# Performance work log

Measured on AMD Instinct MI355X. Metric: run time of the kernel, lower is better.

## Reference

```python
import jax, jax.numpy as jnp
import numpy as np

PI = 3.141592653589793
DET_THRESHOLD = 0.25
MAX_DET = 100
REG_HEAD = 4
DEPTH_MEAN = 28.01  # smoke_coder.depth_ref[0]
DIM_REF = (3.88, 1.63, 1.53)  # smoke_coder.dim_ref[0] (l, h, w)


def setup_inputs() -> dict:
    key = jax.random.key(0)
    k1, k2, k3, k4 = jax.random.split(key, 4)
    B, C, H, W = 32, 3, 256, 832  # stride-4 feature map of 3328x1024 images
    pred_heatmap = jax.random.uniform(k1, (B, C, H, W), dtype=jnp.float32)
    pred_regression = jax.random.normal(k2, (B, C + 1, H, W), dtype=jnp.float32) * 0.1  # REG_HEAD=4 channels
    trans_mat = jnp.tile(jnp.array([[0.25, 0.0, 0.0], [0.0, 0.25, 0.0], [0.0, 0.0, 1.0]], jnp.float32), (B, 1, 1))
    K_mat = jnp.tile(jnp.array([[2100.0, 0.0, 1664.0], [0.0, 2100.0, 512.0], [0.0, 0.0, 1.0]], jnp.float32), (B, 1, 1))
    size = jnp.tile(jnp.array([3328.0, 1024.0], jnp.float32), (B, 1))  # (img_w, img_h)
    h_cam = jax.random.uniform(k3, (B,), jnp.float32, 1.4, 2.0)
    dimensions = jax.random.uniform(k4, (B, 3), jnp.float32, 1.5, 4.0)
    return dict(pred_heatmap=pred_heatmap, pred_regression=pred_regression, trans_mat=trans_mat,
                K_mat=K_mat, size=size, h_cam=h_cam, dimensions=dimensions)


def reference(pred_heatmap, pred_regression, trans_mat, K_mat, size, h_cam, dimensions):
    B, C, H, W = pred_heatmap.shape
    K = MAX_DET
    # ---- nms_hm: 3x3 max-pool, keep local maxima ----
    hmax = jax.lax.reduce_window(pred_heatmap, -jnp.inf, jax.lax.max, (1, 1, 3, 3), (1, 1, 1, 1), 'SAME')
    heat = pred_heatmap * (hmax == pred_heatmap).astype(pred_heatmap.dtype)
    # ---- select_topk: per-class topk then global topk ----
    scores_c, inds_c = jax.lax.top_k(heat.reshape(B, C, H * W), K)  # [B,C,K]
    ys_c = (inds_c // W).astype(jnp.float32)
    xs_c = (inds_c % W).astype(jnp.float32)
    scores, topk_ind = jax.lax.top_k(scores_c.reshape(B, C * K), K)  # [B,K]
    clses = (topk_ind // K).astype(jnp.float32)
    inds = jnp.take_along_axis(inds_c.reshape(B, C * K), topk_ind, axis=1)
    ys = jnp.take_along_axis(ys_c.reshape(B, C * K), topk_ind, axis=1)
    xs = jnp.take_along_axis(xs_c.reshape(B, C * K), topk_ind, axis=1)
    feat = pred_regression.reshape(B, REG_HEAD, H * W).transpose(0, 2, 1)  # [B,HW,R]
    pois = jnp.take_along_axis(feat, inds[:, :, None], axis=1).reshape(-1, REG_HEAD)  # [B*K,R]
    log_dv_delta = pois[:, 0]
    off_u = pois[:, 1]
    ori = pois[:, 2:]
    # ---- feature points -> image points via inverse affine ----
    pts = jnp.stack([xs.reshape(-1), ys.reshape(-1)], axis=1)
    pts = pts + jnp.stack([off_u, jnp.zeros_like(off_u)], axis=1)
    pts_h = jnp.concatenate([pts, jnp.ones((pts.shape[0], 1), pts.dtype)], axis=1)  # [N,3]
    obj = jnp.repeat(jnp.arange(B), K)
    trans_inv = jnp.linalg.inv(trans_mat)[obj]  # [N,3,3]
    img_pts = jnp.einsum('nij,nj->ni', trans_inv, pts_h)[:, :2]
    # ---- per-object camera params ----
    Ks = K_mat[obj]
    h = h_cam[obj]
    kd = dimensions[obj]
    fx, fy, cx = Ks[:, 0, 0], Ks[:, 1, 1], Ks[:, 0, 2]
    dim_ref = jnp.array(DIM_REF, jnp.float32)
    dims = jnp.where(jnp.isfinite(kd), kd, dim_ref[None, :])
    # ---- geometric depth decode ----
    h_ref = h - dims[:, 1] / 2.0
    log_dv_ref = jnp.log(jnp.clip(fy * jnp.abs(h_ref), 1e-7, None) / DEPTH_MEAN)
    log_dv = jnp.clip(log_dv_ref + log_dv_delta, -4.0, 8.0)
    depths = jnp.clip(fy * jnp.abs(h_ref) * jnp.exp(-log_dv), 0.5, 120.0)
    px = (img_pts[:, 0] - cx) * depths / fx
    locs = jnp.stack([px, h, depths], axis=1)  # [N,3]
    # ---- decode_orientation (SMOKE) ----
    rays = jnp.arctan(locs[:, 0] / (locs[:, 2] + 1e-7))
    alphas = jnp.arctan(ori[:, 0] / (ori[:, 1] + 1e-7))
    alphas = alphas + jnp.where(ori[:, 1] >= 0, -PI / 2, PI / 2)
    rotys = alphas + rays
    rotys = jnp.where(rotys > PI, rotys - 2 * PI, rotys)
    rotys = jnp.where(rotys < -PI, rotys + 2 * PI, rotys)
    # ---- encode_box2d: build 3D corners, rotate, project, clamp ----
    cos, sin = jnp.cos(rotys), jnp.sin(rotys)
    cx8 = jnp.array([-0.5, 0.5, 0.5, 0.5, 0.5, -0.5, -0.5, -0.5], jnp.float32)
    cy8 = jnp.array([-1.0, -1.0, 0.0, 0.0, -1.0, -1.0, 0.0, 0.0], jnp.float32)
    cz8 = jnp.array([-0.5, -0.5, -0.5, 0.5, 0.5, 0.5, 0.5, -0.5], jnp.float32)
    xc = dims[:, 0:1] * cx8  # l
    yc = dims[:, 1:2] * cy8  # h
    zc = dims[:, 2:3] * cz8  # w
    bx = cos[:, None] * xc + sin[:, None] * zc
    bz = -sin[:, None] * xc + cos[:, None] * zc
    box3d = jnp.stack([bx, yc, bz], axis=1) + locs[:, :, None]  # [N,3,8]
    proj = jnp.einsum('nij,njk->nik', Ks, box3d)
    uv = proj[:, :2, :] / proj[:, 2:3, :]
    img_w = size.reshape(-1)[0]
    img_h = size.reshape(-1)[1]
    xmins = jnp.clip(jnp.min(uv[:, 0, :], axis=1), 0.0, img_w)
    xmaxs = jnp.clip(jnp.max(uv[:, 0, :], axis=1), 0.0, img_w)
    ymins = jnp.clip(jnp.min(uv[:, 1, :], axis=1), 0.0, img_h)
    ymaxs = jnp.clip(jnp.max(uv[:, 1, :], axis=1), 0.0, img_h)
    box2d = jnp.stack([xmins, ymins, xmaxs, ymaxs], axis=1)
    pred_dims = jnp.roll(dims, -1, axis=1)  # (l,h,w)->(h,w,l)
    result = jnp.concatenate([clses.reshape(-1, 1), alphas[:, None], box2d, pred_dims, locs,
                              rotys[:, None], scores.reshape(-1, 1)], axis=1)  # [N,14]
    # fixed-shape equivalent of boolean filtering: zero out rows below threshold
    keep = (result[:, -1] > DET_THRESHOLD).astype(result.dtype)
    return result * keep[:, None]
```

## Files before the change

kernel.cpp:

```cpp
#include <hip/hip_runtime.h>
#include <math.h>

#define B_ 32
#define C_ 3
#define H_ 256
#define W_ 832
#define HW_ (H_*W_)
#define K_ 100
#define RPB 16
#define PARTS (H_/RPB)
#define NLOAD (W_/4)
#define BLK 256
#define CAP 2048
#define NCAND (C_*PARTS*K_)
#define NB 2048
#define TIE_CAP 128
#define SEL_PASSES 6

typedef unsigned long long ull;
struct DetRec { float score; int cls; unsigned hw; };

template<int N>
__device__ inline void bitonic_sort_desc(ull* s) {
    for (int k = 2; k <= N; k <<= 1) {
        for (int j = k >> 1; j > 0; j >>= 1) {
            __syncthreads();
            for (int i = threadIdx.x; i < N; i += BLK) {
                int ixj = i ^ j;
                if (ixj > i) {
                    ull a = s[i], b = s[ixj];
                    bool up = ((i & k) == 0);
                    if (up ? (a < b) : (a > b)) { s[i] = b; s[ixj] = a; }
                }
            }
        }
    }
    __syncthreads();
}

__device__ inline void find_digit(const unsigned* __restrict__ hist,
                                  unsigned* __restrict__ wtot,
                                  const int kneed,
                                  int* __restrict__ d_s,
                                  int* __restrict__ krem_s,
                                  int* __restrict__ m_s) {
    const int tid = threadIdx.x;
    const int lane = tid & 63;
    const int wid = tid >> 6;
    unsigned l[8];
    unsigned Ls = 0;
    #pragma unroll
    for (int j = 0; j < 8; ++j) { l[j] = hist[tid * 8 + j]; Ls += l[j]; }
    unsigned x = Ls;
    #pragma unroll
    for (int off = 1; off < 64; off <<= 1) {
        unsigned y = __shfl_down(x, off);
        if (lane + off < 64) x += y;
    }
    if (lane == 0) wtot[wid] = x;
    __syncthreads();
    unsigned tail = 0;
    #pragma unroll
    for (int w = 0; w < 4; ++w) if (w > wid) tail += wtot[w];
    unsigned s = x - Ls + tail;
    #pragma unroll
    for (int j = 7; j >= 0; --j) {
        const unsigned Sj = s + l[j];
        if (Sj >= (unsigned)kneed && s < (unsigned)kneed) {
            *d_s = tid * 8 + j;
            *krem_s = kneed - (int)s;
            *m_s = (int)l[j];
        }
        s = Sj;
    }
    __syncthreads();
}

__device__ inline void select_topk(const ull* __restrict__ buf, const int cnt,
                                   ull* __restrict__ dst,
                                   unsigned* __restrict__ hist,
                                   ull* __restrict__ tie,
                                   unsigned* __restrict__ wtot,
                                   int* __restrict__ sh) {
    const int tid = threadIdx.x;
    if (tid == 0) sh[0] = 0;
    int kneed = K_;
    int pshift = 0;
    ull prefix = 0;
    for (int pass = 0; pass < SEL_PASSES; ++pass) {
        const int rs = 53 - 11 * pass;
        const int shift = (rs > 0) ? rs : 0;
        #pragma unroll
        for (int j = 0; j < NB / BLK; ++j) hist[tid + j * BLK] = 0u;
        if (tid == 0) sh[1] = 0;
        __syncthreads();
        for (int i = tid; i < cnt; i += BLK) {
            const ull key = buf[i];
            if (pass > 0 && (key >> pshift) != prefix) continue;
            atomicAdd(&hist[(unsigned)(key >> shift) & 2047u], 1u);
        }
        __syncthreads();
        find_digit(hist, wtot, kneed, &sh[2], &sh[3], &sh[4]);
        const int d = sh[2], krem = sh[3], m = sh[4];
        const bool last = (m <= TIE_CAP) || (pass == SEL_PASSES - 1);
        for (int i = tid; i < cnt; i += BLK) {
            const ull key = buf[i];
            if (pass > 0 && (key >> pshift) != prefix) continue;
            const int dg = (int)((unsigned)(key >> shift) & 2047u);
            if (dg > d) {
                dst[atomicAdd(&sh[0], 1)] = key;
            } else if (last && dg == d) {
                const int p = atomicAdd(&sh[1], 1);
                if (p < TIE_CAP) tie[p] = key;
            }
        }
        __syncthreads();
        if (last) {
            const int n1 = K_ - krem;
            if (sh[1] <= TIE_CAP) {
                const int mm = sh[1];
                for (int i = tid; i < mm; i += BLK) {
                    const ull key = tie[i];
                    int r = 0;
                    for (int j = 0; j < mm; ++j) r += (tie[j] > key) ? 1 : 0;
                    if (r < krem) dst[n1 + r] = key;
                }
            } else {
                for (int i = tid; i < krem; i += BLK) dst[n1 + i] = tie[0];
            }
            __syncthreads();
            return;
        }
        prefix = (prefix << 11) | (ull)(unsigned)d;
        pshift = shift;
        kneed = krem;
    }
}

union TopkShared {
    float vm[2][W_];
    unsigned hist[NB];
};

__global__ void __launch_bounds__(BLK) topk_part_kernel(
        const float* __restrict__ heat, ull* __restrict__ part_out) {
    const int chan = blockIdx.x / PARTS;
    const int c    = chan % C_;
    const int part = blockIdx.x % PARTS;
    const float* __restrict__ hp = heat + (size_t)chan * HW_;
    const int r0 = part * RPB;
    const int tid = threadIdx.x;
    const bool active = tid < NLOAD;
    const int x4 = tid * 4;
    const int lane = tid & 63;

    __shared__ TopkShared sh;
    __shared__ ull buf[CAP];
    __shared__ ull tie[TIE_CAP];
    __shared__ unsigned wtot[4];
    __shared__ int cnt;
    __shared__ int selsh[5];
    if (tid == 0) cnt = 0;

    float4 rA, rB, rC, rD;
    if (active) {
        const int ym1 = (r0 == 0) ? 0 : r0 - 1;
        rA = reinterpret_cast<const float4*>(hp + (size_t)ym1 * W_)[tid];
        rB = reinterpret_cast<const float4*>(hp + (size_t)r0  * W_)[tid];
        const int yp1 = (r0 == H_ - 1) ? r0 : r0 + 1;
        rC = reinterpret_cast<const float4*>(hp + (size_t)yp1 * W_)[tid];
    }
    __syncthreads();

    for (int r = 0; r < RPB; ++r) {
        const int y = r0 + r;
        float* vr = sh.vm[r & 1];
        float4 vm;
        if (active) {
            const int yn = (y + 2 > H_ - 1) ? H_ - 1 : y + 2;
            rD = reinterpret_cast<const float4*>(hp + (size_t)yn * W_)[tid];
            vm.x = fmaxf(fmaxf(rA.x, rB.x), rC.x);
            vm.y = fmaxf(fmaxf(rA.y, rB.y), rC.y);
            vm.z = fmaxf(fmaxf(rA.z, rB.z), rC.z);
            vm.w = fmaxf(fmaxf(rA.w, rB.w), rC.w);
            reinterpret_cast<float4*>(&vr[x4])[0] = vm;
        }
        __syncthreads();
        {
            float left = -INFINITY, right = -INFINITY;
            float vv0 = 0.f, vv1 = 0.f, vv2 = 0.f, vv3 = 0.f;
            if (active) {
                left  = (tid == 0)         ? -INFINITY : vr[x4 - 1];
                right = (tid == NLOAD - 1) ? -INFINITY : vr[x4 + 4];
                vv0 = rB.x; vv1 = rB.y; vv2 = rB.z; vv3 = rB.w;
            }
            const float vn[6] = {left, vm.x, vm.y, vm.z, vm.w, right};
            const float vv[4] = {vv0, vv1, vv2, vv3};
            #pragma unroll
            for (int i = 0; i < 4; ++i) {
                const float v = vv[i];
                const bool peak = active && (v >= vn[i]) && (v >= vn[i+1]) && (v >= vn[i+2]);
                const ull m = __ballot(peak);
                if (peak) {
                    const unsigned p = (unsigned)(y * W_ + x4 + i);
                    const unsigned tiek = ((unsigned)c << 18) | p;
                    const ull key = ((ull)__float_as_uint(v) << 32) | (ull)(~tiek);
                    const int rank = __popcll(m & ((1ULL << lane) - 1ULL));
                    const int leader = __ffsll((long long)m) - 1;
                    int base = 0;
                    if (lane == leader) base = atomicAdd(&cnt, (int)__popcll(m));
                    base = __shfl(base, leader);
                    const int pos = base + rank;
                    if (pos < CAP) buf[pos] = key;
                }
            }
        }
        rA = rB; rB = rC; rC = rD;
    }
    __syncthreads();

    const int cc = (cnt < CAP) ? cnt : CAP;
    ull* o = part_out + (size_t)blockIdx.x * K_;

    if (cc <= K_) {
        for (int i = tid; i < cc; i += BLK) o[i] = buf[i];
        for (int i = cc + tid; i < K_; i += BLK) o[i] = 0ULL;
        return;
    }

    select_topk(buf, cc, o, sh.hist, tie, wtot, selsh);
}

__global__ void __launch_bounds__(BLK) merge_kernel(
        const ull* __restrict__ part_keys, DetRec* __restrict__ dets) {
    const int b = blockIdx.x;
    const int tid = threadIdx.x;
    __shared__ ull buf[NCAND];
    __shared__ unsigned hist[NB];
    __shared__ ull sel[128];
    __shared__ ull tie[TIE_CAP];
    __shared__ unsigned wtot[4];
    __shared__ int selsh[5];
    const ull* src = part_keys + (size_t)b * NCAND;
    for (int i = tid; i < NCAND; i += BLK) buf[i] = src[i];
    if (tid < 128) sel[tid] = 0ULL;
    __syncthreads();

    select_topk(buf, NCAND, sel, hist, tie, wtot, selsh);

    bitonic_sort_desc<128>(sel);

    for (int i = tid; i < K_; i += BLK) {
        const ull key = sel[i];
        const unsigned tiek = ~(unsigned)(key & 0xFFFFFFFFULL);
        DetRec d;
        d.score = __uint_as_float((unsigned)(key >> 32));
        d.cls   = (int)((tiek >> 18) & 3u);
        d.hw    = tiek & 0x3FFFFu;
        dets[(size_t)b * K_ + i] = d;
    }
}

__global__ void __launch_bounds__(BLK) geom_kernel(
        const DetRec* __restrict__ dets, const float* __restrict__ reg,
        const float* __restrict__ trans, const float* __restrict__ Km,
        const float* __restrict__ sz, const float* __restrict__ hcam,
        const float* __restrict__ dimen, float* __restrict__ out) {
    const int n = blockIdx.x * blockDim.x + threadIdx.x;
    if (n >= B_ * K_) return;
    const int b = n / K_;
    DetRec d = dets[n];
    const float score = d.score;
    const float clsf = (float)d.cls;
    unsigned hw = d.hw; if (hw >= HW_) hw = 0;
    const float xs = (float)(hw % W_);
    const float ys = (float)(hw / W_);

    const float* rg = reg + (size_t)b * 4 * HW_;
    const float delta = rg[hw];
    const float off_u = rg[HW_ + hw];
    const float ori0  = rg[2 * HW_ + hw];
    const float ori1  = rg[3 * HW_ + hw];

    const float* T = trans + b * 9;
    const float t00=T[0], t01=T[1], t02=T[2], t10=T[3], t11=T[4], t12=T[5],
                t20=T[6], t21=T[7], t22=T[8];
    const float det3 = t00*(t11*t22 - t12*t21) - t01*(t10*t22 - t12*t20)
                     + t02*(t10*t21 - t11*t20);
    const float idt = 1.0f / det3;
    const float i00 = (t11*t22 - t12*t21)*idt;
    const float i01 = (t02*t21 - t01*t22)*idt;
    const float i02 = (t01*t12 - t02*t11)*idt;

    const float pu = xs + off_u;
    const float img_x = i00*pu + i01*ys + i02;

    const float* Kb = Km + b * 9;
    const float k00=Kb[0],k01=Kb[1],k02=Kb[2],k10=Kb[3],k11=Kb[4],k12=Kb[5],
                k20=Kb[6],k21=Kb[7],k22=Kb[8];
    const float fx = k00, fy = k11, cx = k02;
    const float h = hcam[b];
    float d0 = dimen[b*3+0], d1 = dimen[b*3+1], d2 = dimen[b*3+2];
    if (!isfinite(d0)) d0 = 3.88f;
    if (!isfinite(d1)) d1 = 1.63f;
    if (!isfinite(d2)) d2 = 1.53f;

    const float h_ref = h - d1 * 0.5f;
    const float fyh = fy * fabsf(h_ref);
    const float log_dv_ref = logf(fmaxf(fyh, 1e-7f) / 28.01f);
    const float log_dv = fminf(fmaxf(log_dv_ref + delta, -4.0f), 8.0f);
    const float depth = fminf(fmaxf(fyh * expf(-log_dv), 0.5f), 120.0f);
    const float px = (img_x - cx) * depth / fx;

    const float PI_F  = 3.14159265358979323846f;
    const float ray = atanf(px / (depth + 1e-7f));
    float alpha = atanf(ori0 / (ori1 + 1e-7f));
    alpha += (ori1 >= 0.0f) ? -1.5707963267948966f : 1.5707963267948966f;
    float roty = alpha + ray;
    if (roty >  PI_F) roty -= 6.283185307179586f;
    if (roty < -PI_F) roty += 6.283185307179586f;

    const float cosr = cosf(roty), sinr = sinf(roty);
    const float cx8[8] = {-0.5f, 0.5f, 0.5f, 0.5f, 0.5f,-0.5f,-0.5f,-0.5f};
    const float cy8[8] = {-1.0f,-1.0f, 0.0f, 0.0f,-1.0f,-1.0f, 0.0f, 0.0f};
    const float cz8[8] = {-0.5f,-0.5f,-0.5f, 0.5f, 0.5f, 0.5f, 0.5f,-0.5f};
    float umin = 1e30f, umax = -1e30f, vmin = 1e30f, vmax = -1e30f;
    #pragma unroll
    for (int i = 0; i < 8; ++i) {
        const float xc = d0 * cx8[i];
        const float yc = d1 * cy8[i];
        const float zc = d2 * cz8[i];
        const float X = cosr*xc + sinr*zc + px;
        const float Y = yc + h;
        const float Z = -sinr*xc + cosr*zc + depth;
        const float w = k20*X + k21*Y + k22*Z;
        const float u = (k00*X + k01*Y + k02*Z) / w;
        const float v = (k10*X + k11*Y + k12*Z) / w;
        umin = fminf(umin, u); umax = fmaxf(umax, u);
        vmin = fminf(vmin, v); vmax = fmaxf(vmax, v);
    }
    const float img_w = sz[0], img_h = sz[1];
    const float xmin = fminf(fmaxf(umin, 0.0f), img_w);
    const float xmax = fminf(fmaxf(umax, 0.0f), img_w);
    const float ymin = fminf(fmaxf(vmin, 0.0f), img_h);
    const float ymax = fminf(fmaxf(vmax, 0.0f), img_h);

    const float keep = (score > 0.25f) ? 1.0f : 0.0f;
    float* o = out + (size_t)n * 14;
    o[0]  = clsf  * keep;
    o[1]  = alpha * keep;
    o[2]  = xmin  * keep;
    o[3]  = ymin  * keep;
    o[4]  = xmax  * keep;
    o[5]  = ymax  * keep;
    o[6]  = d1    * keep;
    o[7]  = d2    * keep;
    o[8]  = d0    * keep;
    o[9]  = px    * keep;
    o[10] = h     * keep;
    o[11] = depth * keep;
    o[12] = roty  * keep;
    o[13] = score * keep;
}

extern "C" void kernel_launch(void* const* d_in, const int* in_sizes, int n_in,
                              void* d_out, int out_size, void* d_ws, size_t ws_size,
                              hipStream_t stream) {
    const float* heat  = (const float*)d_in[0];
    const float* reg   = (const float*)d_in[1];
    const float* trans = (const float*)d_in[2];
    const float* Kmat  = (const float*)d_in[3];
    const float* sz    = (const float*)d_in[4];
    const float* hcam  = (const float*)d_in[5];
    const float* dimen = (const float*)d_in[6];
    float* out = (float*)d_out;

    char* ws = (char*)d_ws;
    ull* part_keys = (ull*)ws;
    ws += (size_t)B_ * C_ * PARTS * K_ * sizeof(ull);
    DetRec* dets = (DetRec*)ws;

    topk_part_kernel<<<B_ * C_ * PARTS, BLK, 0, stream>>>(heat, part_keys);
    merge_kernel<<<B_, BLK, 0, stream>>>(part_keys, dets);
    geom_kernel<<<(B_ * K_ + BLK - 1) / BLK, BLK, 0, stream>>>(
        dets, reg, trans, Kmat, sz, hcam, dimen, out);
}
```

Baseline: 245.0 us.

## Use wave shuffles for horizontal max and fuse merge with geometry kernel

The topk partition kernel now gets horizontal neighbours of the vertical max from wave shuffles, with lane 0 and lane 63 loading halo columns directly from global memory. This removes the shared-memory staging buffer and the per-row __syncthreads. Separately, the merge kernel now computes the geometry output itself, which drops one kernel launch and the intermediate detection records. The fused geometry runs on only 32 blocks of 100 threads each, so it gets less parallelism than the separate kernel had.

```diff
diff --git a/kernel.cpp b/kernel.cpp
--- a/kernel.cpp
+++ b/kernel.cpp
@@ -18,7 +18,6 @@
 #define SEL_PASSES 6
 
 typedef unsigned long long ull;
-struct DetRec { float score; int cls; unsigned hw; };
 
 template<int N>
 __device__ inline void bitonic_sort_desc(ull* s) {
@@ -137,11 +136,6 @@
     }
 }
 
-union TopkShared {
-    float vm[2][W_];
-    unsigned hist[NB];
-};
-
 __global__ void __launch_bounds__(BLK) topk_part_kernel(
         const float* __restrict__ heat, ull* __restrict__ part_out) {
     const int chan = blockIdx.x / PARTS;
@@ -154,7 +148,7 @@
     const int x4 = tid * 4;
     const int lane = tid & 63;
 
-    __shared__ TopkShared sh;
+    __shared__ unsigned hist[NB];
     __shared__ ull buf[CAP];
     __shared__ ull tie[TIE_CAP];
     __shared__ unsigned wtot[4];
@@ -162,44 +156,60 @@
     __shared__ int selsh[5];
     if (tid == 0) cnt = 0;
 
+    const bool needL = active && (lane == 0) && (tid > 0);
+    const bool needR = active && (lane == 63);
+
     float4 rA, rB, rC, rD;
+    float aL = 0.f, bL = 0.f, cL = 0.f, dL = 0.f;
+    float aR = 0.f, bR = 0.f, cR = 0.f, dR = 0.f;
+    {
+        const int ym1 = (r0 == 0) ? 0 : r0 - 1;
+        const int yp1 = (r0 == H_ - 1) ? r0 : r0 + 1;
+        if (active) {
+            rA = reinterpret_cast<const float4*>(hp + (size_t)ym1 * W_)[tid];
+            rB = reinterpret_cast<const float4*>(hp + (size_t)r0  * W_)[tid];
+            rC = reinterpret_cast<const float4*>(hp + (size_t)yp1 * W_)[tid];
+        }
+        if (needL) {
+            aL = hp[(size_t)ym1 * W_ + x4 - 1];
+            bL = hp[(size_t)r0  * W_ + x4 - 1];
+            cL = hp[(size_t)yp1 * W_ + x4 - 1];
+        }
+        if (needR) {
+            aR = hp[(size_t)ym1 * W_ + x4 + 4];
+            bR = hp[(size_t)r0  * W_ + x4 + 4];
+            cR = hp[(size_t)yp1 * W_ + x4 + 4];
+        }
+    }
+    __syncthreads();
+
     if (active) {
-        const int ym1 = (r0 == 0) ? 0 : r0 - 1;
-        rA = reinterpret_cast<const float4*>(hp + (size_t)ym1 * W_)[tid];
-        rB = reinterpret_cast<const float4*>(hp + (size_t)r0  * W_)[tid];
-        const int yp1 = (r0 == H_ - 1) ? r0 : r0 + 1;
-        rC = reinterpret_cast<const float4*>(hp + (size_t)yp1 * W_)[tid];
-    }
-    __syncthreads();
-
-    for (int r = 0; r < RPB; ++r) {
-        const int y = r0 + r;
-        float* vr = sh.vm[r & 1];
-        float4 vm;
-        if (active) {
+        for (int r = 0; r < RPB; ++r) {
+            const int y = r0 + r;
             const int yn = (y + 2 > H_ - 1) ? H_ - 1 : y + 2;
             rD = reinterpret_cast<const float4*>(hp + (size_t)yn * W_)[tid];
+            if (needL) dL = hp[(size_t)yn * W_ + x4 - 1];
+            if (needR) dR = hp[(size_t)yn * W_ + x4 + 4];
+
+            float4 vm;
             vm.x = fmaxf(fmaxf(rA.x, rB.x), rC.x);
             vm.y = fmaxf(fmaxf(rA.y, rB.y), rC.y);
             vm.z = fmaxf(fmaxf(rA.z, rB.z), rC.z);
             vm.w = fmaxf(fmaxf(rA.w, rB.w), rC.w);
-            reinterpret_cast<float4*>(&vr[x4])[0] = vm;
-        }
-        __syncthreads();
-        {
-            float left = -INFINITY, right = -INFINITY;
-            float vv0 = 0.f, vv1 = 0.f, vv2 = 0.f, vv3 = 0.f;
-            if (active) {
-                left  = (tid == 0)         ? -INFINITY : vr[x4 - 1];
-                right = (tid == NLOAD - 1) ? -INFINITY : vr[x4 + 4];
-                vv0 = rB.x; vv1 = rB.y; vv2 = rB.z; vv3 = rB.w;
-            }
+            const float lmax = needL ? fmaxf(fmaxf(aL, bL), cL) : -INFINITY;
+            const float rmax = needR ? fmaxf(fmaxf(aR, bR), cR) : -INFINITY;
+
+            float left  = __shfl_up(vm.w, 1);
+            float right = __shfl_down(vm.x, 1);
+            if (lane == 0) left = lmax;
+            if (lane == 63 || tid == NLOAD - 1) right = rmax;
+
             const float vn[6] = {left, vm.x, vm.y, vm.z, vm.w, right};
-            const float vv[4] = {vv0, vv1, vv2, vv3};
+            const float vv[4] = {rB.x, rB.y, rB.z, rB.w};
             #pragma unroll
             for (int i = 0; i < 4; ++i) {
                 const float v = vv[i];
-                const bool peak = active && (v >= vn[i]) && (v >= vn[i+1]) && (v >= vn[i+2]);
+                const bool peak = (v >= vn[i]) && (v >= vn[i+1]) && (v >= vn[i+2]);
                 const ull m = __ballot(peak);
                 if (peak) {
                     const unsigned p = (unsigned)(y * W_ + x4 + i);
@@ -214,8 +224,10 @@
                     if (pos < CAP) buf[pos] = key;
                 }
             }
-        }
-        rA = rB; rB = rC; rC = rD;
+            rA = rB; rB = rC; rC = rD;
+            aL = bL; bL = cL; cL = dL;
+            aR = bR; bR = cR; cR = dR;
+        }
     }
     __syncthreads();
 
@@ -228,11 +240,14 @@
         return;
     }
 
-    select_topk(buf, cc, o, sh.hist, tie, wtot, selsh);
-}
-
-__global__ void __launch_bounds__(BLK) merge_kernel(
-        const ull* __restrict__ part_keys, DetRec* __restrict__ dets) {
+    select_topk(buf, cc, o, hist, tie, wtot, selsh);
+}
+
+__global__ void __launch_bounds__(BLK) merge_geom_kernel(
+        const ull* __restrict__ part_keys, const float* __restrict__ reg,
+        const float* __restrict__ trans, const float* __restrict__ Km,
+        const float* __restrict__ sz, const float* __restrict__ hcam,
+        const float* __restrict__ dimen, float* __restrict__ out) {
     const int b = blockIdx.x;
     const int tid = threadIdx.x;
     __shared__ ull buf[NCAND];
@@ -253,114 +268,99 @@
     for (int i = tid; i < K_; i += BLK) {
         const ull key = sel[i];
         const unsigned tiek = ~(unsigned)(key & 0xFFFFFFFFULL);
-        DetRec d;
-        d.score = __uint_as_float((unsigned)(key >> 32));
-        d.cls   = (int)((tiek >> 18) & 3u);
-        d.hw    = tiek & 0x3FFFFu;
-        dets[(size_t)b * K_ + i] = d;
-    }
-}
-
-__global__ void __launch_bounds__(BLK) geom_kernel(
-        const DetRec* __restrict__ dets, const float* __restrict__ reg,
-        const float* __restrict__ trans, const float* __restrict__ Km,
-        const float* __restrict__ sz, const float* __restrict__ hcam,
-        const float* __restrict__ dimen, float* __restrict__ out) {
-    const int n = blockIdx.x * blockDim.x + threadIdx.x;
-    if (n >= B_ * K_) return;
-    const int b = n / K_;
-    DetRec d = dets[n];
-    const float score = d.score;
-    const float clsf = (float)d.cls;
-    unsigned hw = d.hw; if (hw >= HW_) hw = 0;
-    const float xs = (float)(hw % W_);
-    const float ys = (float)(hw / W_);
-
-    const float* rg = reg + (size_t)b * 4 * HW_;
-    const float delta = rg[hw];
-    const float off_u = rg[HW_ + hw];
-    const float ori0  = rg[2 * HW_ + hw];
-    const float ori1  = rg[3 * HW_ + hw];
-
-    const float* T = trans + b * 9;
-    const float t00=T[0], t01=T[1], t02=T[2], t10=T[3], t11=T[4], t12=T[5],
-                t20=T[6], t21=T[7], t22=T[8];
-    const float det3 = t00*(t11*t22 - t12*t21) - t01*(t10*t22 - t12*t20)
-                     + t02*(t10*t21 - t11*t20);
-    const float idt = 1.0f / det3;
-    const float i00 = (t11*t22 - t12*t21)*idt;
-    const float i01 = (t02*t21 - t01*t22)*idt;
-    const float i02 = (t01*t12 - t02*t11)*idt;
-
-    const float pu = xs + off_u;
-    const float img_x = i00*pu + i01*ys + i02;
-
-    const float* Kb = Km + b * 9;
-    const float k00=Kb[0],k01=Kb[1],k02=Kb[2],k10=Kb[3],k11=Kb[4],k12=Kb[5],
-                k20=Kb[6],k21=Kb[7],k22=Kb[8];
-    const float fx = k00, fy = k11, cx = k02;
-    const float h = hcam[b];
-    float d0 = dimen[b*3+0], d1 = dimen[b*3+1], d2 = dimen[b*3+2];
-    if (!isfinite(d0)) d0 = 3.88f;
-    if (!isfinite(d1)) d1 = 1.63f;
-    if (!isfinite(d2)) d2 = 1.53f;
-
-    const float h_ref = h - d1 * 0.5f;
-    const float fyh = fy * fabsf(h_ref);
-    const float log_dv_ref = logf(fmaxf(fyh, 1e-7f) / 28.01f);
-    const float log_dv = fminf(fmaxf(log_dv_ref + delta, -4.0f), 8.0f);
-    const float depth = fminf(fmaxf(fyh * expf(-log_dv), 0.5f), 120.0f);
-    const float px = (img_x - cx) * depth / fx;
-
-    const float PI_F  = 3.14159265358979323846f;
-    const float ray = atanf(px / (depth + 1e-7f));
-    float alpha = atanf(ori0 / (ori1 + 1e-7f));
-    alpha += (ori1 >= 0.0f) ? -1.5707963267948966f : 1.5707963267948966f;
-    float roty = alpha + ray;
-    if (roty >  PI_F) roty -= 6.283185307179586f;
-    if (roty < -PI_F) roty += 6.283185307179586f;
-
-    const float cosr = cosf(roty), sinr = sinf(roty);
-    const float cx8[8] = {-0.5f, 0.5f, 0.5f, 0.5f, 0.5f,-0.5f,-0.5f,-0.5f};
-    const float cy8[8] = {-1.0f,-1.0f, 0.0f, 0.0f,-1.0f,-1.0f, 0.0f, 0.0f};
-    const float cz8[8] = {-0.5f,-0.5f,-0.5f, 0.5f, 0.5f, 0.5f, 0.5f,-0.5f};
-    float umin = 1e30f, umax = -1e30f, vmin = 1e30f, vmax = -1e30f;
-    #pragma unroll
-    for (int i = 0; i < 8; ++i) {
-        const float xc = d0 * cx8[i];
-        const float yc = d1 * cy8[i];
-        const float zc = d2 * cz8[i];
-        const float X = cosr*xc + sinr*zc + px;
-        const float Y = yc + h;
-        const float Z = -sinr*xc + cosr*zc + depth;
-        const float w = k20*X + k21*Y + k22*Z;
-        const float u = (k00*X + k01*Y + k02*Z) / w;
-        const float v = (k10*X + k11*Y + k12*Z) / w;
-        umin = fminf(umin, u); umax = fmaxf(umax, u);
-        vmin = fminf(vmin, v); vmax = fmaxf(vmax, v);
-    }
-    const float img_w = sz[0], img_h = sz[1];
-    const float xmin = fminf(fmaxf(umin, 0.0f), img_w);
-    const float xmax = fminf(fmaxf(umax, 0.0f), img_w);
-    const float ymin = fminf(fmaxf(vmin, 0.0f), img_h);
-    const float ymax = fminf(fmaxf(vmax, 0.0f), img_h);
-
-    const float keep = (score > 0.25f) ? 1.0f : 0.0f;
-    float* o = out + (size_t)n * 14;
-    o[0]  = clsf  * keep;
-    o[1]  = alpha * keep;
-    o[2]  = xmin  * keep;
-    o[3]  = ymin  * keep;
-    o[4]  = xmax  * keep;
-    o[5]  = ymax  * keep;
-    o[6]  = d1    * keep;
-    o[7]  = d2    * keep;
-    o[8]  = d0    * keep;
-    o[9]  = px    * keep;
-    o[10] = h     * keep;
-    o[11] = depth * keep;
-    o[12] = roty  * keep;
-    o[13] = score * keep;
+        const float score = __uint_as_float((unsigned)(key >> 32));
+        const float clsf = (float)((tiek >> 18) & 3u);
+        unsigned hw = tiek & 0x3FFFFu;
+        if (hw >= HW_) hw = 0;
+        const float xs = (float)(hw % W_);
+        const float ys = (float)(hw / W_);
+
+        const float* rg = reg + (size_t)b * 4 * HW_;
+        const float delta = rg[hw];
+        const float off_u = rg[HW_ + hw];
+        const float ori0  = rg[2 * HW_ + hw];
+        const float ori1  = rg[3 * HW_ + hw];
+
+        const float* T = trans + b * 9;
+        const float t00=T[0], t01=T[1], t02=T[2], t10=T[3], t11=T[4], t12=T[5],
+                    t20=T[6], t21=T[7], t22=T[8];
+        const float det3 = t00*(t11*t22 - t12*t21) - t01*(t10*t22 - t12*t20)
+                         + t02*(t10*t21 - t11*t20);
+        const float idt = 1.0f / det3;
+        const float i00 = (t11*t22 - t12*t21)*idt;
+        const float i01 = (t02*t21 - t01*t22)*idt;
+        const float i02 = (t01*t12 - t02*t11)*idt;
+
+        const float pu = xs + off_u;
+        const float img_x = i00*pu + i01*ys + i02;
+
+        const float* Kb = Km + b * 9;
+        const float k00=Kb[0],k01=Kb[1],k02=Kb[2],k10=Kb[3],k11=Kb[4],k12=Kb[5],
+                    k20=Kb[6],k21=Kb[7],k22=Kb[8];
+        const float fx = k00, fy = k11, cx = k02;
+        const float h = hcam[b];
+        float d0 = dimen[b*3+0], d1 = dimen[b*3+1], d2 = dimen[b*3+2];
+        if (!isfinite(d0)) d0 = 3.88f;
+        if (!isfinite(d1)) d1 = 1.63f;
+        if (!isfinite(d2)) d2 = 1.53f;
+
+        const float h_ref = h - d1 * 0.5f;
+        const float fyh = fy * fabsf(h_ref);
+        const float log_dv_ref = logf(fmaxf(fyh, 1e-7f) / 28.01f);
+        const float log_dv = fminf(fmaxf(log_dv_ref + delta, -4.0f), 8.0f);
+        const float depth = fminf(fmaxf(fyh * expf(-log_dv), 0.5f), 120.0f);
+        const float px = (img_x - cx) * depth / fx;
+
+        const float PI_F  = 3.14159265358979323846f;
+        const float ray = atanf(px / (depth + 1e-7f));
+        float alpha = atanf(ori0 / (ori1 + 1e-7f));
+        alpha += (ori1 >= 0.0f) ? -1.5707963267948966f : 1.5707963267948966f;
+        float roty = alpha + ray;
+        if (roty >  PI_F) roty -= 6.283185307179586f;
+        if (roty < -PI_F) roty += 6.283185307179586f;
+
+        const float cosr = cosf(roty), sinr = sinf(roty);
+        const float cx8[8] = {-0.5f, 0.5f, 0.5f, 0.5f, 0.5f,-0.5f,-0.5f,-0.5f};
+        const float cy8[8] = {-1.0f,-1.0f, 0.0f, 0.0f,-1.0f,-1.0f, 0.0f, 0.0f};
+        const float cz8[8] = {-0.5f,-0.5f,-0.5f, 0.5f, 0.5f, 0.5f, 0.5f,-0.5f};
+        float umin = 1e30f, umax = -1e30f, vmin = 1e30f, vmax = -1e30f;
+        #pragma unroll
+        for (int j = 0; j < 8; ++j) {
+            const float xc = d0 * cx8[j];
+            const float yc = d1 * cy8[j];
+            const float zc = d2 * cz8[j];
+            const float X = cosr*xc + sinr*zc + px;
+            const float Y = yc + h;
+            const float Z = -sinr*xc + cosr*zc + depth;
+            const float w = k20*X + k21*Y + k22*Z;
+            const float u = (k00*X + k01*Y + k02*Z) / w;
+            const float v = (k10*X + k11*Y + k12*Z) / w;
+            umin = fminf(umin, u); umax = fmaxf(umax, u);
+            vmin = fminf(vmin, v); vmax = fmaxf(vmax, v);
+        }
+        const float img_w = sz[0], img_h = sz[1];
+        const float xmin = fminf(fmaxf(umin, 0.0f), img_w);
+        const float xmax = fminf(fmaxf(umax, 0.0f), img_w);
+        const float ymin = fminf(fmaxf(vmin, 0.0f), img_h);
+        const float ymax = fminf(fmaxf(vmax, 0.0f), img_h);
+
+        const float keep = (score > 0.25f) ? 1.0f : 0.0f;
+        float* o = out + (size_t)(b * K_ + i) * 14;
+        o[0]  = clsf  * keep;
+        o[1]  = alpha * keep;
+        o[2]  = xmin  * keep;
+        o[3]  = ymin  * keep;
+        o[4]  = xmax  * keep;
+        o[5]  = ymax  * keep;
+        o[6]  = d1    * keep;
+        o[7]  = d2    * keep;
+        o[8]  = d0    * keep;
+        o[9]  = px    * keep;
+        o[10] = h     * keep;
+        o[11] = depth * keep;
+        o[12] = roty  * keep;
+        o[13] = score * keep;
+    }
 }
 
 extern "C" void kernel_launch(void* const* d_in, const int* in_sizes, int n_in,
@@ -375,13 +375,9 @@
     const float* dimen = (const float*)d_in[6];
     float* out = (float*)d_out;
 
-    char* ws = (char*)d_ws;
-    ull* part_keys = (ull*)ws;
-    ws += (size_t)B_ * C_ * PARTS * K_ * sizeof(ull);
-    DetRec* dets = (DetRec*)ws;
+    ull* part_keys = (ull*)d_ws;
 
     topk_part_kernel<<<B_ * C_ * PARTS, BLK, 0, stream>>>(heat, part_keys);
-    merge_kernel<<<B_, BLK, 0, stream>>>(part_keys, dets);
-    geom_kernel<<<(B_ * K_ + BLK - 1) / BLK, BLK, 0, stream>>>(
-        dets, reg, trans, Kmat, sz, hcam, dimen, out);
-}
+    merge_geom_kernel<<<B_, BLK, 0, stream>>>(
+        part_keys, reg, trans, Kmat, sz, hcam, dimen, out);
+}
```

Measured after the change: 241.4 us. Within noise of the previous version (-1.5%).
